# Kernel optimization log

Hardware: AMD Instinct MI355X
Metric: run time of the kernel (lower is better)

The kernel has to match this reference:

```python
import jax, jax.numpy as jnp
import numpy as np

N = 20000      # nodes
E1 = 100000    # topo (2d) edges
E2 = 100000    # distance edges
HID = 128      # hidden_size
N2D = 128      # node_embed_size_2d
E2D = 64       # edge_embed_size_2d
EF = 128       # edge_feat_size
ET = 32        # edge_type_size
NRBF = 64
CUT = 6.0


def rbf_expand(d):
    # Gaussian radial basis with cosine cutoff envelope, d: [E]
    centers = jnp.linspace(0.0, CUT, NRBF)
    width = CUT / NRBF
    env = 0.5 * (jnp.cos(jnp.pi * jnp.clip(d / CUT, 0.0, 1.0)) + 1.0)
    return jnp.exp(-((d[:, None] - centers) ** 2) / (2.0 * width * width)) * env[:, None]


def setup_inputs() -> dict:
    key = jax.random.key(0)
    ks = jax.random.split(key, 20)
    s = 0.02
    return {
        "H": jax.random.normal(ks[0], (N, HID), jnp.float32),
        "V": jax.random.normal(ks[1], (N, HID, 3), jnp.float32),
        "Z": jax.random.normal(ks[2], (N, 3), jnp.float32) * 3.0,
        "layer_i": 0,
        "H_2d": jax.random.normal(ks[3], (N, N2D), jnp.float32),
        "mask_2d": jnp.ones((N,), bool),
        "E2d_idx": jax.random.randint(ks[4], (2, E1), 0, N),
        "E2d_feat": jax.random.normal(ks[5], (E2D, E1), jnp.float32),
        "Z_3d": jax.random.normal(ks[6], (N, 3), jnp.float32) * 3.0,
        "mask_3d": jnp.ones((N,), bool),
        "Edist_idx": jax.random.randint(ks[7], (2, E2), 0, N),
        "Edist_val": jax.random.uniform(ks[8], (E2,), jnp.float32) * CUT,
        "virtual_node_embed": jax.random.normal(ks[9], (1, N2D), jnp.float32),
        "edge_type_embed": jax.random.normal(ks[10], (3, ET), jnp.float32),
        "W_rbf": jax.random.normal(ks[11], (EF, NRBF), jnp.float32) * s,
        "W_e2d": jax.random.normal(ks[12], (EF, E2D), jnp.float32) * s,
        "W_i": jax.random.normal(ks[13], (HID, HID + N2D), jnp.float32) * s,
        "W_phi1": jax.random.normal(ks[14], (HID, HID + EF + ET), jnp.float32) * s,
        "b_phi1": jnp.zeros((HID,), jnp.float32),
        "W_phi2": jax.random.normal(ks[15], (3 * HID, HID), jnp.float32) * s,
        "b_phi2": jnp.zeros((3 * HID,), jnp.float32),
        "W_msg": jax.random.normal(ks[16], (3 * HID, NRBF), jnp.float32) * s,
        "b_msg": jnp.zeros((3 * HID,), jnp.float32),
    }


def reference(H, V, Z, layer_i, H_2d, mask_2d, E2d_idx, E2d_feat, Z_3d, mask_3d,
              Edist_idx, Edist_val, virtual_node_embed, edge_type_embed,
              W_rbf, W_e2d, W_i, W_phi1, b_phi1, W_phi2, b_phi2, W_msg, b_msg):
    n = H.shape[0]
    # mask_3d is all-True in this fixture => n_cond_3d == n (static shapes)
    nodes_real = jnp.concatenate([H, H_2d], axis=-1)                       # [n, h1+h2]
    virt = jnp.broadcast_to(virtual_node_embed, (n, virtual_node_embed.shape[1]))
    nodes_virt = jnp.concatenate([H, virt], axis=-1)                        # [n, h1+h2]
    nodes = jnp.concatenate([nodes_real, nodes_virt], axis=0) @ W_i.T      # [2n, h1]
    v = jnp.concatenate([V, jnp.zeros_like(V)], axis=0)                     # [2n, h1, 3]
    z = jnp.concatenate([Z, Z_3d], axis=0)                                  # [2n, 3]

    row_3d = jnp.arange(n)
    col_3d = jnp.arange(n) + n
    E3d = jnp.stack([jnp.concatenate([row_3d, col_3d]),
                     jnp.concatenate([col_3d, row_3d])], axis=0)            # [2, 2n]
    edges = jnp.concatenate([E2d_idx, E3d, Edist_idx], axis=-1)             # [2, E]
    e1, e3, e2 = E2d_idx.shape[1], E3d.shape[1], Edist_idx.shape[1]
    edge_type = jnp.concatenate([jnp.zeros((e1,), jnp.int32),
                                 jnp.ones((e3,), jnp.int32),
                                 jnp.full((e2,), 2, jnp.int32)])
    et = edge_type_embed[edge_type]                                         # [E, ET]
    attr2d = E2d_feat.T @ W_e2d.T                                           # [e1, EF]
    attr3d = jnp.zeros((e3, W_e2d.shape[0]), jnp.float32)                   # [e3, EF]
    attrd = rbf_expand(Edist_val) @ W_rbf.T                                 # [e2, EF]
    edge_attr = jnp.concatenate(
        [jnp.concatenate([attr2d, attr3d, attrd], axis=0), et], axis=-1)    # [E, EF+ET]

    # AdapterLayer: PaiNN-style equivariant message passing
    row, col = edges[0], edges[1]
    rel = z[row] - z[col]                                                   # [E, 3]
    dist = jnp.sqrt(jnp.sum(rel * rel, axis=-1) + 1e-8)                     # [E]
    unit = rel / dist[:, None]
    phi_in = jnp.concatenate([nodes[col], edge_attr], axis=-1)
    phi = jax.nn.silu(phi_in @ W_phi1.T + b_phi1) @ W_phi2.T + b_phi2       # [E, 3h]
    wd = rbf_expand(dist) @ W_msg.T + b_msg                                 # [E, 3h]
    m = phi * wd
    h = nodes.shape[1]
    s_msg, v_gate, r_gate = m[:, :h], m[:, h:2 * h], m[:, 2 * h:]
    dv = v[col] * v_gate[:, :, None] + unit[:, None, :] * r_gate[:, :, None]  # [E, h, 3]
    nn2 = nodes.shape[0]
    H_add = jax.ops.segment_sum(s_msg, row, num_segments=nn2)[:n]
    V_add = jax.ops.segment_sum(dv, row, num_segments=nn2)[:n]

    # eval-mode clamp
    H_add = jnp.clip(H_add, -100.0, 100.0)
    V_add = jnp.clip(V_add, -100.0, 100.0)

    mask_dist = jnp.zeros((n,), bool).at[Edist_idx[0]].set(True).at[Edist_idx[1]].set(True)
    update_mask = mask_2d | mask_3d | mask_dist
    H_add = jnp.where(update_mask[:, None], H_add, 0.0)
    V_add = jnp.where(update_mask[:, None, None], V_add, 0.0)
    return H_add, V_add
```

## Files before the change

### kernel.cpp

```cpp
#include <hip/hip_runtime.h>
#include <hip/hip_bf16.h>

#define NN   20000
#define E1N  100000
#define E2N  100000
#define NEFF 220000
#define TILE 64
#define NBLK ((NEFF + TILE - 1) / TILE)
#define NPAD (NBLK * TILE)
#define RBF_STEP   0.09523809523809523f
#define RBF_INV2W2 56.88888888888889f

typedef short  bf16x8 __attribute__((ext_vector_type(8)));
typedef float  f32x4  __attribute__((ext_vector_type(4)));

__device__ __forceinline__ float4 ld4(const float* p) {
    return *reinterpret_cast<const float4*>(p);
}
__device__ __forceinline__ ushort f2bf(float x) {
    __hip_bfloat16 h = __float2bfloat16(x);
    return *reinterpret_cast<ushort*>(&h);
}
__device__ __forceinline__ float bf2f(ushort u) {
    return __uint_as_float(((unsigned)u) << 16);
}
__device__ __forceinline__ float env_of(float d) {
    float x = fminf(fmaxf(d * (1.0f / 6.0f), 0.0f), 1.0f);
    return 0.5f * (__cosf(3.14159265358979f * x) + 1.0f);
}

__device__ __forceinline__ int edge_row(int eid, const int* __restrict__ E2d_idx,
                                        const int* __restrict__ Edist_idx) {
    if (eid < E1N) return E2d_idx[eid];
    if (eid < E1N + NN) return eid - E1N;
    return Edist_idx[eid - E1N - NN];
}

__global__ __launch_bounds__(256) void hist_kernel(
    const int* __restrict__ E2d_idx, const int* __restrict__ Edist_idx,
    int* __restrict__ hist) {
    int g = blockIdx.x * 256 + threadIdx.x;
    if (g < NEFF) atomicAdd(&hist[edge_row(g, E2d_idx, Edist_idx)], 1);
}

__global__ __launch_bounds__(1024) void scan_kernel(
    const int* __restrict__ hist, int* __restrict__ start, int* __restrict__ cursor) {
    __shared__ int buf[1024];
    __shared__ int carry;
    const int t = threadIdx.x;
    if (t == 0) carry = 0;
    __syncthreads();
    for (int chunk = 0; chunk < 20; ++chunk) {
        int idx = chunk * 1024 + t;
        int v = (idx < NN) ? hist[idx] : 0;
        buf[t] = v;
        __syncthreads();
        for (int off = 1; off < 1024; off <<= 1) {
            int x = (t >= off) ? buf[t - off] : 0;
            __syncthreads();
            buf[t] += x;
            __syncthreads();
        }
        int excl  = buf[t] - v;
        int cbase = carry;
        int tot   = buf[1023];
        if (idx <= NN) {
            start[idx] = cbase + excl;
            if (idx < NN) cursor[idx] = cbase + excl;
        }
        __syncthreads();
        if (t == 0) carry = cbase + tot;
        __syncthreads();
    }
}

__global__ __launch_bounds__(256) void scatter_kernel(
    const int* __restrict__ E2d_idx, const int* __restrict__ Edist_idx,
    int* __restrict__ cursor, int* __restrict__ order) {
    int g = blockIdx.x * 256 + threadIdx.x;
    if (g < NEFF) {
        int r = edge_row(g, E2d_idx, Edist_idx);
        int pos = atomicAdd(&cursor[r], 1);
        order[pos] = g;
    }
}

__global__ __launch_bounds__(64) void chunkrow_kernel(
    const int* __restrict__ order, const int* __restrict__ E2d_idx,
    const int* __restrict__ Edist_idx, int cap, int nch, int* __restrict__ chunk_r0) {
    int i = threadIdx.x;
    if (i < nch) {
        int p = i * cap;
        if (p >= NEFF) p = NEFF - 1;
        chunk_r0[i] = edge_row(order[p], E2d_idx, Edist_idx);
    }
}

__global__ __launch_bounds__(256) void meta_kernel(
    const int* __restrict__ order, const int* __restrict__ E2d_idx,
    const int* __restrict__ Edist_idx, const float* __restrict__ Edist_val,
    const float* __restrict__ Z, const float* __restrict__ Z3d,
    int4* __restrict__ metaI, float4* __restrict__ metaF,
    float4* __restrict__ payloadU) {
    int g = blockIdx.x * 256 + threadIdx.x;
    if (g >= NPAD) return;
    int eid = (g < NEFF) ? order[g] : -1;
    int row, col, ty, e2 = 0; float dval = 0.f;
    if (eid < 0)             { ty = 1; row = -1; col = 0; }
    else if (eid < E1N)      { ty = 0; row = E2d_idx[eid]; col = E2d_idx[E1N + eid]; e2 = eid; }
    else if (eid < E1N + NN) { ty = 1; int jj = eid - E1N; row = jj; col = jj + NN; }
    else { ty = 2; int g2 = eid - E1N - NN;
           row = Edist_idx[g2]; col = Edist_idx[E2N + g2]; dval = Edist_val[g2]; }
    int rs = (row < 0) ? 0 : row;
    float prx = Z[rs * 3], pry = Z[rs * 3 + 1], prz = Z[rs * 3 + 2];
    float pcx, pcy, pcz;
    if (col < NN) { pcx = Z[col * 3]; pcy = Z[col * 3 + 1]; pcz = Z[col * 3 + 2]; }
    else { int c = col - NN; pcx = Z3d[c * 3]; pcy = Z3d[c * 3 + 1]; pcz = Z3d[c * 3 + 2]; }
    float dx = prx - pcx, dy = pry - pcy, dz = prz - pcz;
    float dist = sqrtf(dx * dx + dy * dy + dz * dz + 1e-8f);
    float inv = 1.0f / dist;
    int vcol = (col < NN) ? col : -1;
    metaI[g] = make_int4(col, row, ty, e2);
    metaF[g] = make_float4(dist, dval, env_of(dist), env_of(dval));
    if (row >= 0)
        payloadU[g] = make_float4(dx * inv, dy * inv, dz * inv, __int_as_float(vcol));
}

__global__ __launch_bounds__(256) void prep_kernel(
    const float* __restrict__ W_phi1, const float* __restrict__ b_phi1,
    const float* __restrict__ W_e2d, const float* __restrict__ W_rbf,
    const float* __restrict__ W_phi2, const float* __restrict__ W_msg,
    const float* __restrict__ et, const float* __restrict__ W_i,
    ushort* __restrict__ W1c, ushort* __restrict__ W2b,
    ushort* __restrict__ Wmb, float* __restrict__ b_type,
    ushort* __restrict__ Wib) {
    int g = blockIdx.x * 256 + threadIdx.x;
    if (g < 32768) {
        int n = g >> 8, k = g & 255;
        float v;
        if (k < 128) v = W_phi1[n * 288 + k];
        else {
            int kk = k - 128;
            const float* Wsel = (kk < 64) ? W_e2d : W_rbf;
            int j = kk & 63;
            float s = 0.f;
            for (int a = 0; a < 128; ++a) s += W_phi1[n * 288 + 128 + a] * Wsel[a * 64 + j];
            v = s;
        }
        W1c[n * 256 + k] = f2bf(v);
    } else if (g < 81920) {
        int q = g - 32768; W2b[q] = f2bf(W_phi2[q]);
    } else if (g < 106496) {
        int q = g - 81920; Wmb[q] = f2bf(W_msg[q]);
    } else if (g < 106880) {
        int q = g - 106496; int ty = q >> 7, n = q & 127;
        float s = b_phi1[n];
        for (int a = 0; a < 32; ++a) s += W_phi1[n * 288 + 256 + a] * et[ty * 32 + a];
        b_type[q] = s;
    } else if (g < 139648) {
        int q = g - 106880; Wib[q] = f2bf(W_i[q]);
    }
}

__global__ __launch_bounds__(256) void featT_kernel(
    const float* __restrict__ feat, ushort* __restrict__ featTb) {
    __shared__ float tile[64][65];
    const int t = threadIdx.x;
    const int cbase = blockIdx.x * 64;
    for (int i = t; i < 64 * 64; i += 256) {
        int k = i >> 6, e = i & 63;
        tile[k][e] = (cbase + e < E1N) ? feat[(size_t)k * E1N + cbase + e] : 0.f;
    }
    __syncthreads();
    for (int i = t; i < 64 * 64; i += 256) {
        int e = i >> 6, k = i & 63;
        if (cbase + e < E1N) featTb[(size_t)(cbase + e) * 64 + k] = f2bf(tile[k][e]);
    }
}

__global__ __launch_bounds__(256, 2) void nodes_mfma_kernel(
    const float* __restrict__ H, const float* __restrict__ H2d,
    const float* __restrict__ virt, const ushort* __restrict__ Wib,
    ushort* __restrict__ nodesb) {
    __shared__ ushort A[64][264];
    __shared__ ushort WB[128][132];

    const int t = threadIdx.x;
    const int gbase = blockIdx.x * 64;

    for (int i = t; i < 64 * 64; i += 256) {
        int e = i >> 6, q = i & 63;
        int row = gbase + e;
        float4 v;
        if (q < 32)          v = ld4(H + (size_t)((row < NN) ? row : row - NN) * 128 + q * 4);
        else if (row < NN)   v = ld4(H2d + (size_t)row * 128 + (q - 32) * 4);
        else                 v = ld4(virt + (q - 32) * 4);
        ushort tmp[4] = {f2bf(v.x), f2bf(v.y), f2bf(v.z), f2bf(v.w)};
        *reinterpret_cast<uint2*>(&A[e][q * 4]) = *reinterpret_cast<const uint2*>(tmp);
    }
    for (int i = t; i < 128 * 16; i += 256) {
        int n = i >> 4, q = i & 15;
        *reinterpret_cast<uint4*>(&WB[n][q * 8]) =
            *reinterpret_cast<const uint4*>(Wib + (size_t)n * 256 + q * 8);
    }
    __syncthreads();

    const int w  = t >> 6, lane = t & 63;
    const int mh = w >> 1, nh = w & 1;
    const int lr = lane >> 4, lc = lane & 15;
    const int ar0 = mh * 32 + lc;

    f32x4 acc[2][4];
#pragma unroll
    for (int mt = 0; mt < 2; ++mt)
#pragma unroll
        for (int nt = 0; nt < 4; ++nt) acc[mt][nt] = (f32x4){0.f, 0.f, 0.f, 0.f};
#pragma unroll
    for (int ks = 0; ks < 4; ++ks) {
        bf16x8 a0 = *reinterpret_cast<const bf16x8*>(&A[ar0][ks * 32 + lr * 8]);
        bf16x8 a1 = *reinterpret_cast<const bf16x8*>(&A[ar0 + 16][ks * 32 + lr * 8]);
#pragma unroll
        for (int nt = 0; nt < 4; ++nt) {
            int n = nh * 64 + nt * 16 + lc;
            bf16x8 b = *reinterpret_cast<const bf16x8*>(&WB[n][ks * 32 + lr * 8]);
            acc[0][nt] = __builtin_amdgcn_mfma_f32_16x16x32_bf16(a0, b, acc[0][nt], 0, 0, 0);
            acc[1][nt] = __builtin_amdgcn_mfma_f32_16x16x32_bf16(a1, b, acc[1][nt], 0, 0, 0);
        }
    }
    __syncthreads();
    for (int i = t; i < 128 * 16; i += 256) {
        int n = i >> 4, q = i & 15;
        *reinterpret_cast<uint4*>(&WB[n][q * 8]) =
            *reinterpret_cast<const uint4*>(Wib + (size_t)n * 256 + 128 + q * 8);
    }
    __syncthreads();
#pragma unroll
    for (int ks = 4; ks < 8; ++ks) {
        bf16x8 a0 = *reinterpret_cast<const bf16x8*>(&A[ar0][ks * 32 + lr * 8]);
        bf16x8 a1 = *reinterpret_cast<const bf16x8*>(&A[ar0 + 16][ks * 32 + lr * 8]);
#pragma unroll
        for (int nt = 0; nt < 4; ++nt) {
            int n = nh * 64 + nt * 16 + lc;
            bf16x8 b = *reinterpret_cast<const bf16x8*>(&WB[n][(ks - 4) * 32 + lr * 8]);
            acc[0][nt] = __builtin_amdgcn_mfma_f32_16x16x32_bf16(a0, b, acc[0][nt], 0, 0, 0);
            acc[1][nt] = __builtin_amdgcn_mfma_f32_16x16x32_bf16(a1, b, acc[1][nt], 0, 0, 0);
        }
    }
#pragma unroll
    for (int mt = 0; mt < 2; ++mt)
#pragma unroll
        for (int nt = 0; nt < 4; ++nt)
#pragma unroll
            for (int r = 0; r < 4; ++r) {
                int e  = mh * 32 + mt * 16 + lr * 4 + r;
                int ch = nh * 64 + nt * 16 + lc;
                nodesb[(size_t)(gbase + e) * 128 + ch] = f2bf(acc[mt][nt][r]);
            }
}

template <int MODE>
__global__ __launch_bounds__(256, 2) void edge_kernel(
    const ushort* __restrict__ nodesb, const float* __restrict__ V,
    const float* __restrict__ Z, const float* __restrict__ Z3d,
    const int* __restrict__ E2d_idx, const float* __restrict__ E2d_feat,
    const ushort* __restrict__ featTb,
    const int* __restrict__ Edist_idx, const float* __restrict__ Edist_val,
    const ushort* __restrict__ W1c, const ushort* __restrict__ W2b,
    const ushort* __restrict__ Wmb, const float* __restrict__ b_type,
    const float* __restrict__ b_phi2, const float* __restrict__ b_msg,
    const int4* __restrict__ metaI, const float4* __restrict__ metaF,
    int p0, ushort* __restrict__ payloadM,
    float* __restrict__ Hout, float* __restrict__ Vout) {

    __shared__ ushort A1f[TILE * 264 + 256];
    __shared__ ushort WB[128][132];
    __shared__ float  s_bt[3][128];
    __shared__ int    s_row[TILE], s_col[TILE], s_ty[TILE], s_e2[TILE], s_vcol[TILE];
    __shared__ float  s_dist[TILE], s_dval[TILE], s_env[TILE], s_env2[TILE];
    __shared__ float  s_unit[TILE][3];

    ushort* hidp  = A1f;
    ushort* m_lds = A1f + 8704;

    const int t = threadIdx.x;
    const int gbase = blockIdx.x * TILE;

    if (MODE == 1) {
        if (t < TILE) {
            int4 mi = metaI[p0 + gbase + t];
            s_col[t] = mi.x; s_row[t] = mi.y; s_ty[t] = mi.z; s_e2[t] = mi.w;
        } else if (t < 2 * TILE) {
            int e = t - TILE;
            float4 mf = metaF[p0 + gbase + e];
            s_dist[e] = mf.x; s_dval[e] = mf.y; s_env[e] = mf.z; s_env2[e] = mf.w;
        }
    } else {
        if (t < TILE) {
            int gpos = gbase + t;
            int eid = (gpos < NEFF) ? gpos : -1;
            int row, col, ty, e2 = 0; float dval = 0.f;
            if (eid < 0)             { ty = 1; row = -1; col = 0; }
            else if (eid < E1N)      { ty = 0; row = E2d_idx[eid]; col = E2d_idx[E1N + eid]; e2 = eid; }
            else if (eid < E1N + NN) { ty = 1; int jj = eid - E1N; row = jj; col = jj + NN; }
            else { ty = 2; int g2 = eid - E1N - NN;
                   row = Edist_idx[g2]; col = Edist_idx[E2N + g2]; dval = Edist_val[g2]; }
            int rs = (row < 0) ? 0 : row;
            float prx = Z[rs * 3], pry = Z[rs * 3 + 1], prz = Z[rs * 3 + 2];
            float pcx, pcy, pcz;
            if (col < NN) { pcx = Z[col * 3]; pcy = Z[col * 3 + 1]; pcz = Z[col * 3 + 2]; }
            else { int c = col - NN; pcx = Z3d[c * 3]; pcy = Z3d[c * 3 + 1]; pcz = Z3d[c * 3 + 2]; }
            float dx = prx - pcx, dy = pry - pcy, dz = prz - pcz;
            float dist = sqrtf(dx * dx + dy * dy + dz * dz + 1e-8f);
            float inv = 1.0f / dist;
            s_row[t] = row; s_col[t] = col; s_ty[t] = ty; s_e2[t] = e2;
            s_vcol[t] = (col < NN) ? col : -1;
            s_unit[t][0] = dx * inv; s_unit[t][1] = dy * inv; s_unit[t][2] = dz * inv;
            s_dist[t] = dist; s_dval[t] = dval;
            s_env[t] = env_of(dist); s_env2[t] = env_of(dval);
        }
    }
    for (int i = t; i < 384; i += 256) ((float*)s_bt)[i] = b_type[i];
    __syncthreads();

    for (int i = t; i < TILE * 16; i += 256) {
        int e = i >> 4, q = i & 15;
        *reinterpret_cast<uint4*>(&A1f[e * 264 + q * 8]) =
            *reinterpret_cast<const uint4*>(nodesb + (size_t)s_col[e] * 128 + q * 8);
    }
    if (MODE == 1) {
        for (int i = t; i < TILE * 128; i += 256) {
            int e = i >> 7, k = i & 127;
            int ty = s_ty[e];
            ushort v = 0;
            if (ty == 0) { if (k < 64) v = featTb[(size_t)s_e2[e] * 64 + k]; }
            else if (ty == 2) {
                if (k >= 64) {
                    float dd = s_dval[e] - (float)(k - 64) * RBF_STEP;
                    v = f2bf(__expf(-dd * dd * RBF_INV2W2) * s_env2[e]);
                }
            }
            A1f[e * 264 + 128 + k] = v;
        }
    } else {
        for (int i = t; i < TILE * 128; i += 256) {
            int k = i >> 6, e = i & 63;
            int ty = s_ty[e];
            float v = 0.f;
            if (ty == 0) { if (k < 64) v = E2d_feat[(size_t)k * E1N + s_e2[e]]; }
            else if (ty == 2) {
                if (k >= 64) {
                    float dd = s_dval[e] - (float)(k - 64) * RBF_STEP;
                    v = __expf(-dd * dd * RBF_INV2W2) * s_env2[e];
                }
            }
            A1f[e * 264 + 128 + k] = f2bf(v);
        }
    }
    for (int i = t; i < 128 * 16; i += 256) {
        int n = i >> 4, q = i & 15;
        *reinterpret_cast<uint4*>(&WB[n][q * 8]) =
            *reinterpret_cast<const uint4*>(W1c + (size_t)n * 256 + q * 8);
    }
    __syncthreads();

    const int w  = t >> 6, lane = t & 63;
    const int mh = w >> 1, nh = w & 1;
    const int lr = lane >> 4, lc = lane & 15;
    const int ar0 = mh * 32 + lc;

    bf16x8 ra0[2], ra1[2];
    {
        float dA = s_dist[ar0],      eA = s_env[ar0];
        float dB = s_dist[ar0 + 16], eB = s_env[ar0 + 16];
#pragma unroll
        for (int ks = 0; ks < 2; ++ks)
#pragma unroll
            for (int j = 0; j < 8; ++j) {
                float c  = (float)(ks * 32 + lr * 8 + j) * RBF_STEP;
                float tA = dA - c, tB = dB - c;
                ra0[ks][j] = (short)f2bf(__expf(-tA * tA * RBF_INV2W2) * eA);
                ra1[ks][j] = (short)f2bf(__expf(-tB * tB * RBF_INV2W2) * eB);
            }
    }

    f32x4 acc[2][4];
#pragma unroll
    for (int mt = 0; mt < 2; ++mt)
#pragma unroll
        for (int nt = 0; nt < 4; ++nt) acc[mt][nt] = (f32x4){0.f, 0.f, 0.f, 0.f};
#pragma unroll
    for (int ks = 0; ks < 4; ++ks) {
        bf16x8 a0 = *reinterpret_cast<const bf16x8*>(&A1f[ar0 * 264 + ks * 32 + lr * 8]);
        bf16x8 a1 = *reinterpret_cast<const bf16x8*>(&A1f[(ar0 + 16) * 264 + ks * 32 + lr * 8]);
#pragma unroll
        for (int nt = 0; nt < 4; ++nt) {
            int n = nh * 64 + nt * 16 + lc;
            bf16x8 b = *reinterpret_cast<const bf16x8*>(&WB[n][ks * 32 + lr * 8]);
            acc[0][nt] = __builtin_amdgcn_mfma_f32_16x16x32_bf16(a0, b, acc[0][nt], 0, 0, 0);
            acc[1][nt] = __builtin_amdgcn_mfma_f32_16x16x32_bf16(a1, b, acc[1][nt], 0, 0, 0);
        }
    }
    __syncthreads();
    for (int i = t; i < 128 * 16; i += 256) {
        int n = i >> 4, q = i & 15;
        *reinterpret_cast<uint4*>(&WB[n][q * 8]) =
            *reinterpret_cast<const uint4*>(W1c + (size_t)n * 256 + 128 + q * 8);
    }
    __syncthreads();
#pragma unroll
    for (int ks = 4; ks < 8; ++ks) {
        bf16x8 a0 = *reinterpret_cast<const bf16x8*>(&A1f[ar0 * 264 + ks * 32 + lr * 8]);
        bf16x8 a1 = *reinterpret_cast<const bf16x8*>(&A1f[(ar0 + 16) * 264 + ks * 32 + lr * 8]);
#pragma unroll
        for (int nt = 0; nt < 4; ++nt) {
            int n = nh * 64 + nt * 16 + lc;
            bf16x8 b = *reinterpret_cast<const bf16x8*>(&WB[n][(ks - 4) * 32 + lr * 8]);
            acc[0][nt] = __builtin_amdgcn_mfma_f32_16x16x32_bf16(a0, b, acc[0][nt], 0, 0, 0);
            acc[1][nt] = __builtin_amdgcn_mfma_f32_16x16x32_bf16(a1, b, acc[1][nt], 0, 0, 0);
        }
    }
    __syncthreads();

#pragma unroll
    for (int mt = 0; mt < 2; ++mt)
#pragma unroll
        for (int nt = 0; nt < 4; ++nt)
#pragma unroll
            for (int r = 0; r < 4; ++r) {
                int e  = mh * 32 + mt * 16 + lr * 4 + r;
                int ch = nh * 64 + nt * 16 + lc;
                float x = acc[mt][nt][r] + s_bt[s_ty[e]][ch];
                hidp[e * 136 + ch] = f2bf(x / (1.0f + __expf(-x)));
            }
    for (int i = t; i < 128 * 16; i += 256) {
        int n = i >> 4, q = i & 15;
        *reinterpret_cast<uint4*>(&WB[n][q * 8]) =
            *reinterpret_cast<const uint4*>(W2b + (size_t)n * 128 + q * 8);
    }
    __syncthreads();

    bf16x8 ha0[4], ha1[4];
#pragma unroll
    for (int ks = 0; ks < 4; ++ks) {
        ha0[ks] = *reinterpret_cast<const bf16x8*>(&hidp[ar0 * 136 + ks * 32 + lr * 8]);
        ha1[ks] = *reinterpret_cast<const bf16x8*>(&hidp[(ar0 + 16) * 136 + ks * 32 + lr * 8]);
    }

    f32x4 vgr[2][4];
#pragma unroll
    for (int c = 0; c < 3; ++c) {
        f32x4 p[2][4], g[2][4];
#pragma unroll
        for (int mt = 0; mt < 2; ++mt)
#pragma unroll
            for (int nt = 0; nt < 4; ++nt) {
                p[mt][nt] = (f32x4){0.f, 0.f, 0.f, 0.f};
                g[mt][nt] = (f32x4){0.f, 0.f, 0.f, 0.f};
            }
#pragma unroll
        for (int ks = 0; ks < 4; ++ks) {
#pragma unroll
            for (int nt = 0; nt < 4; ++nt) {
                int n = nh * 64 + nt * 16 + lc;
                bf16x8 b = *reinterpret_cast<const bf16x8*>(&WB[n][ks * 32 + lr * 8]);
                p[0][nt] = __builtin_amdgcn_mfma_f32_16x16x32_bf16(ha0[ks], b, p[0][nt], 0, 0, 0);
                p[1][nt] = __builtin_amdgcn_mfma_f32_16x16x32_bf16(ha1[ks], b, p[1][nt], 0, 0, 0);
            }
        }
#pragma unroll
        for (int ks = 0; ks < 2; ++ks) {
#pragma unroll
            for (int nt = 0; nt < 4; ++nt) {
                int n = c * 128 + nh * 64 + nt * 16 + lc;
                bf16x8 b = *reinterpret_cast<const bf16x8*>(Wmb + (size_t)n * 64 + ks * 32 + lr * 8);
                g[0][nt] = __builtin_amdgcn_mfma_f32_16x16x32_bf16(ra0[ks], b, g[0][nt], 0, 0, 0);
                g[1][nt] = __builtin_amdgcn_mfma_f32_16x16x32_bf16(ra1[ks], b, g[1][nt], 0, 0, 0);
            }
        }
        __syncthreads();
        if (c < 2) {
            for (int i = t; i < 128 * 16; i += 256) {
                int n = i >> 4, q = i & 15;
                *reinterpret_cast<uint4*>(&WB[n][q * 8]) =
                    *reinterpret_cast<const uint4*>(W2b + (size_t)((c + 1) * 128 + n) * 128 + q * 8);
            }
        }
#pragma unroll
        for (int mt = 0; mt < 2; ++mt)
#pragma unroll
            for (int nt = 0; nt < 4; ++nt) {
                int d  = nh * 64 + nt * 16 + lc;
                float b2 = b_phi2[c * 128 + d];
                float bm = b_msg[c * 128 + d];
#pragma unroll
                for (int r = 0; r < 4; ++r) {
                    int e = mh * 32 + mt * 16 + lr * 4 + r;
                    float m = (p[mt][nt][r] + b2) * (g[mt][nt][r] + bm);
                    if (MODE == 1) {
                        m_lds[e * 132 + d] = f2bf(m);
                    } else {
                        int row = s_row[e];
                        if (c == 0) {
                            if (row >= 0) unsafeAtomicAdd(&Hout[(size_t)row * 128 + d], m);
                        } else if (c == 1) {
                            vgr[mt][nt][r] = m;
                        } else if (row >= 0) {
                            float vgv = vgr[mt][nt][r];
                            int vc = s_vcol[e];
                            float vx = 0.f, vy = 0.f, vz = 0.f;
                            if (vc >= 0) {
                                const float* vp = V + ((size_t)vc * 128 + d) * 3;
                                vx = vp[0]; vy = vp[1]; vz = vp[2];
                            }
                            float* vo = Vout + ((size_t)row * 128 + d) * 3;
                            unsafeAtomicAdd(vo + 0, vx * vgv + s_unit[e][0] * m);
                            unsafeAtomicAdd(vo + 1, vy * vgv + s_unit[e][1] * m);
                            unsafeAtomicAdd(vo + 2, vz * vgv + s_unit[e][2] * m);
                        }
                    }
                }
            }
        __syncthreads();
        if (MODE == 1) {
            for (int i = t; i < 2048; i += 256) {
                int e = i >> 5, q = i & 31;
                *reinterpret_cast<uint2*>(payloadM + (size_t)(gbase + e) * 384 + c * 128 + q * 4) =
                    *reinterpret_cast<const uint2*>(m_lds + e * 132 + q * 4);
            }
        }
    }
}

__global__ __launch_bounds__(256) void reduce_kernel(
    const ushort* __restrict__ payloadM, const float4* __restrict__ payloadU,
    const float* __restrict__ V, const int* __restrict__ start,
    const int* __restrict__ chunk_r0, int ci, int p0, int p1,
    float* __restrict__ Hout, float* __restrict__ Vout) {
    const int t = threadIdx.x;
    const int rbase = chunk_r0[ci] + blockIdx.x * 8;
    const bool hside = (t < 128);
    const int d = hside ? t : (t - 128);
    for (int nr = 0; nr < 8; ++nr) {
        int r = rbase + nr;
        if (r >= NN) return;
        int s0 = start[r], s1 = start[r + 1];
        if (s0 >= p1) return;
        int a = (s0 > p0) ? s0 : p0;
        int b = (s1 < p1) ? s1 : p1;
        if (a >= b) continue;
        int n = b - a;
        if (hside) {
            const ushort* base = payloadM + (size_t)(a - p0) * 384 + d;
            float a0 = 0.f, a1 = 0.f, a2 = 0.f, a3 = 0.f;
            int i = 0;
            for (; i + 4 <= n; i += 4) {
                a0 += bf2f(base[(size_t)i * 384]);
                a1 += bf2f(base[(size_t)(i + 1) * 384]);
                a2 += bf2f(base[(size_t)(i + 2) * 384]);
                a3 += bf2f(base[(size_t)(i + 3) * 384]);
            }
            for (; i < n; ++i) a0 += bf2f(base[(size_t)i * 384]);
            float acc = (a0 + a1) + (a2 + a3);
            float* ptr = &Hout[(size_t)r * 128 + d];
            float o = *ptr + acc;
            if (s1 <= p1) o = fminf(fmaxf(o, -100.f), 100.f);
            *ptr = o;
        } else {
            const ushort* base = payloadM + (size_t)(a - p0) * 384;
            const float4* ub = payloadU + a;
            float ax = 0.f, ay = 0.f, az = 0.f;
            float bx = 0.f, by = 0.f, bz = 0.f;
            int i = 0;
            for (; i + 2 <= n; i += 2) {
                const ushort* pm0 = base + (size_t)i * 384;
                const ushort* pm1 = base + (size_t)(i + 1) * 384;
                float vg0 = bf2f(pm0[128 + d]), rg0 = bf2f(pm0[256 + d]);
                float vg1 = bf2f(pm1[128 + d]), rg1 = bf2f(pm1[256 + d]);
                float4 u0 = ub[i];
                float4 u1 = ub[i + 1];
                int vc0 = __float_as_int(u0.w);
                int vc1 = __float_as_int(u1.w);
                if (vc0 >= 0) {
                    const float* vp = V + (size_t)vc0 * 384 + d * 3;
                    ax += vg0 * vp[0]; ay += vg0 * vp[1]; az += vg0 * vp[2];
                }
                if (vc1 >= 0) {
                    const float* vp = V + (size_t)vc1 * 384 + d * 3;
                    bx += vg1 * vp[0]; by += vg1 * vp[1]; bz += vg1 * vp[2];
                }
                ax += rg0 * u0.x; ay += rg0 * u0.y; az += rg0 * u0.z;
                bx += rg1 * u1.x; by += rg1 * u1.y; bz += rg1 * u1.z;
            }
            if (i < n) {
                const ushort* pm0 = base + (size_t)i * 384;
                float vg0 = bf2f(pm0[128 + d]), rg0 = bf2f(pm0[256 + d]);
                float4 u0 = ub[i];
                int vc0 = __float_as_int(u0.w);
                if (vc0 >= 0) {
                    const float* vp = V + (size_t)vc0 * 384 + d * 3;
                    ax += vg0 * vp[0]; ay += vg0 * vp[1]; az += vg0 * vp[2];
                }
                ax += rg0 * u0.x; ay += rg0 * u0.y; az += rg0 * u0.z;
            }
            ax += bx; ay += by; az += bz;
            float* vo = Vout + (size_t)r * 384 + d * 3;
            float ox = vo[0] + ax, oy = vo[1] + ay, oz = vo[2] + az;
            if (s1 <= p1) {
                ox = fminf(fmaxf(ox, -100.f), 100.f);
                oy = fminf(fmaxf(oy, -100.f), 100.f);
                oz = fminf(fmaxf(oz, -100.f), 100.f);
            }
            vo[0] = ox; vo[1] = oy; vo[2] = oz;
        }
    }
}

extern "C" void kernel_launch(void* const* d_in, const int* in_sizes, int n_in,
                              void* d_out, int out_size, void* d_ws, size_t ws_size,
                              hipStream_t stream) {
    const float* H         = (const float*)d_in[0];
    const float* V         = (const float*)d_in[1];
    const float* Z         = (const float*)d_in[2];
    const float* H2d       = (const float*)d_in[4];
    const int*   E2d_idx   = (const int*)d_in[6];
    const float* E2d_feat  = (const float*)d_in[7];
    const float* Z3d       = (const float*)d_in[8];
    const int*   Edist_idx = (const int*)d_in[10];
    const float* Edist_val = (const float*)d_in[11];
    const float* virt      = (const float*)d_in[12];
    const float* et        = (const float*)d_in[13];
    const float* W_rbf     = (const float*)d_in[14];
    const float* W_e2d     = (const float*)d_in[15];
    const float* W_i       = (const float*)d_in[16];
    const float* W_phi1    = (const float*)d_in[17];
    const float* b_phi1    = (const float*)d_in[18];
    const float* W_phi2    = (const float*)d_in[19];
    const float* b_phi2    = (const float*)d_in[20];
    const float* W_msg     = (const float*)d_in[21];
    const float* b_msg     = (const float*)d_in[22];

    ushort* nodesb  = (ushort*)d_ws;
    ushort* W1c     = nodesb + 5120000;
    ushort* W2b     = W1c + 32768;
    ushort* Wmb     = W2b + 49152;
    ushort* Wib     = Wmb + 24576;
    float*  b_type  = (float*)(Wib + 32768);
    ushort* featTb  = (ushort*)(b_type + 384);
    int*    hist    = (int*)(featTb + (size_t)E1N * 64);
    int*    cursor  = hist + NN;
    int*    start   = cursor + NN;
    int*    order   = start + NN + 1;
    int*    chunk_r0= order + NPAD;
    int4*   metaI   = (int4*)(((size_t)(chunk_r0 + 64) + 15) & ~(size_t)15);
    float4* metaF   = (float4*)(metaI + NPAD);
    float4* payloadU= metaF + NPAD;

    size_t fixed = (size_t)((char*)(payloadU + NPAD) - (char*)d_ws);
    size_t poff  = (fixed + 255) & ~(size_t)255;
    size_t avail = (ws_size > poff) ? (ws_size - poff) : 0;
    long long cap_ll = (long long)(avail / 768) / TILE * TILE;
    int cap = (cap_ll > (long long)NPAD) ? NPAD : (int)cap_ll;
    const bool big = (cap >= 4096);
    ushort* payloadM = (ushort*)((char*)d_ws + poff);

    float* Hout = (float*)d_out;
    float* Vout = Hout + (size_t)NN * 128;

    hipMemsetAsync(d_out, 0, (size_t)out_size * sizeof(float), stream);
    prep_kernel<<<(139648 + 255) / 256, 256, 0, stream>>>(
        W_phi1, b_phi1, W_e2d, W_rbf, W_phi2, W_msg, et, W_i,
        W1c, W2b, Wmb, b_type, Wib);
    nodes_mfma_kernel<<<(2 * NN) / 64, 256, 0, stream>>>(H, H2d, virt, Wib, nodesb);

    if (big) {
        hipMemsetAsync(hist, 0, NN * sizeof(int), stream);
        featT_kernel<<<(E1N + 63) / 64, 256, 0, stream>>>(E2d_feat, featTb);
        hist_kernel<<<(NEFF + 255) / 256, 256, 0, stream>>>(E2d_idx, Edist_idx, hist);
        scan_kernel<<<1, 1024, 0, stream>>>(hist, start, cursor);
        scatter_kernel<<<(NEFF + 255) / 256, 256, 0, stream>>>(E2d_idx, Edist_idx, cursor, order);
        meta_kernel<<<(NPAD + 255) / 256, 256, 0, stream>>>(
            order, E2d_idx, Edist_idx, Edist_val, Z, Z3d, metaI, metaF, payloadU);
        int bpc = cap / TILE;
        int nch = (NBLK + bpc - 1) / bpc;
        chunkrow_kernel<<<1, 64, 0, stream>>>(order, E2d_idx, Edist_idx, cap, nch, chunk_r0);
        int rbound = (NN < cap + 1) ? NN : (cap + 1);
        int rgrid  = (rbound + 7) / 8;
        for (int ci = 0; ci < nch; ++ci) {
            int b0 = ci * bpc;
            int nb = ((NBLK - b0) < bpc) ? (NBLK - b0) : bpc;
            int p0 = b0 * TILE;
            int p1 = p0 + nb * TILE; if (p1 > NEFF) p1 = NEFF;
            edge_kernel<1><<<nb, 256, 0, stream>>>(
                nodesb, V, Z, Z3d, E2d_idx, E2d_feat, featTb, Edist_idx, Edist_val,
                W1c, W2b, Wmb, b_type, b_phi2, b_msg, metaI, metaF, p0, payloadM,
                Hout, Vout);
            reduce_kernel<<<rgrid, 256, 0, stream>>>(payloadM, payloadU, V, start,
                                                     chunk_r0, ci, p0, p1, Hout, Vout);
        }
    } else {
        edge_kernel<0><<<NBLK, 256, 0, stream>>>(
            nodesb, V, Z, Z3d, E2d_idx, E2d_feat, featTb, Edist_idx, Edist_val,
            W1c, W2b, Wmb, b_type, b_phi2, b_msg, metaI, metaF, 0, payloadM,
            Hout, Vout);
    }
}
```

Before: 405.2 us.

## Fuse segmented row reduction into edge kernel, drop payload buffer and reduce pass

The separate reduce_kernel and its chunk loop are removed. The edge kernel now sums messages for consecutive same-row edges inside each sorted tile, reading from LDS planes. It writes a row directly when the row lies entirely within the tile and uses atomics at tile boundaries. This avoids writing and re-reading a large bf16 message payload in global memory and removes many kernel launches. The cost is serial per-thread reduction loops run by only half the block, and rows that span tiles are accumulated by atomics without the final clamp.

Result: slower. 512.5 us (+26.5%).

```diff
diff --git a/kernel.cpp b/kernel.cpp
--- a/kernel.cpp
+++ b/kernel.cpp
@@ -27,6 +27,9 @@
 __device__ __forceinline__ float env_of(float d) {
     float x = fminf(fmaxf(d * (1.0f / 6.0f), 0.0f), 1.0f);
     return 0.5f * (__cosf(3.14159265358979f * x) + 1.0f);
+}
+__device__ __forceinline__ float clip100(float x) {
+    return fminf(fmaxf(x, -100.f), 100.f);
 }
 
 __device__ __forceinline__ int edge_row(int eid, const int* __restrict__ E2d_idx,
@@ -85,23 +88,12 @@
     }
 }
 
-__global__ __launch_bounds__(64) void chunkrow_kernel(
-    const int* __restrict__ order, const int* __restrict__ E2d_idx,
-    const int* __restrict__ Edist_idx, int cap, int nch, int* __restrict__ chunk_r0) {
-    int i = threadIdx.x;
-    if (i < nch) {
-        int p = i * cap;
-        if (p >= NEFF) p = NEFF - 1;
-        chunk_r0[i] = edge_row(order[p], E2d_idx, Edist_idx);
-    }
-}
-
 __global__ __launch_bounds__(256) void meta_kernel(
     const int* __restrict__ order, const int* __restrict__ E2d_idx,
     const int* __restrict__ Edist_idx, const float* __restrict__ Edist_val,
     const float* __restrict__ Z, const float* __restrict__ Z3d,
     int4* __restrict__ metaI, float4* __restrict__ metaF,
-    float4* __restrict__ payloadU) {
+    float4* __restrict__ metaU) {
     int g = blockIdx.x * 256 + threadIdx.x;
     if (g >= NPAD) return;
     int eid = (g < NEFF) ? order[g] : -1;
@@ -122,8 +114,9 @@
     int vcol = (col < NN) ? col : -1;
     metaI[g] = make_int4(col, row, ty, e2);
     metaF[g] = make_float4(dist, dval, env_of(dist), env_of(dval));
-    if (row >= 0)
-        payloadU[g] = make_float4(dx * inv, dy * inv, dz * inv, __int_as_float(vcol));
+    metaU[g] = (row >= 0)
+        ? make_float4(dx * inv, dy * inv, dz * inv, __int_as_float(vcol))
+        : make_float4(0.f, 0.f, 0.f, __int_as_float(-1));
 }
 
 __global__ __launch_bounds__(256) void prep_kernel(
@@ -269,7 +262,7 @@
     const ushort* __restrict__ Wmb, const float* __restrict__ b_type,
     const float* __restrict__ b_phi2, const float* __restrict__ b_msg,
     const int4* __restrict__ metaI, const float4* __restrict__ metaF,
-    int p0, ushort* __restrict__ payloadM,
+    const float4* __restrict__ metaU, const int* __restrict__ start,
     float* __restrict__ Hout, float* __restrict__ Vout) {
 
     __shared__ ushort A1f[TILE * 264 + 256];
@@ -279,19 +272,24 @@
     __shared__ float  s_dist[TILE], s_dval[TILE], s_env[TILE], s_env2[TILE];
     __shared__ float  s_unit[TILE][3];
 
-    ushort* hidp  = A1f;
-    ushort* m_lds = A1f + 8704;
+    ushort* hidp   = A1f;
+    ushort* plane0 = A1f;
+    ushort* plane1 = A1f + 8448;
 
     const int t = threadIdx.x;
     const int gbase = blockIdx.x * TILE;
+    const int pg = gbase;
 
     if (MODE == 1) {
         if (t < TILE) {
-            int4 mi = metaI[p0 + gbase + t];
+            int4 mi = metaI[gbase + t];
             s_col[t] = mi.x; s_row[t] = mi.y; s_ty[t] = mi.z; s_e2[t] = mi.w;
+            float4 u = metaU[gbase + t];
+            s_unit[t][0] = u.x; s_unit[t][1] = u.y; s_unit[t][2] = u.z;
+            s_vcol[t] = __float_as_int(u.w);
         } else if (t < 2 * TILE) {
             int e = t - TILE;
-            float4 mf = metaF[p0 + gbase + e];
+            float4 mf = metaF[gbase + e];
             s_dist[e] = mf.x; s_dval[e] = mf.y; s_env[e] = mf.z; s_env2[e] = mf.w;
         }
     } else {
@@ -478,27 +476,130 @@
             }
         }
         __syncthreads();
-        if (c < 2) {
-            for (int i = t; i < 128 * 16; i += 256) {
-                int n = i >> 4, q = i & 15;
-                *reinterpret_cast<uint4*>(&WB[n][q * 8]) =
-                    *reinterpret_cast<const uint4*>(W2b + (size_t)((c + 1) * 128 + n) * 128 + q * 8);
-            }
-        }
-#pragma unroll
-        for (int mt = 0; mt < 2; ++mt)
-#pragma unroll
-            for (int nt = 0; nt < 4; ++nt) {
-                int d  = nh * 64 + nt * 16 + lc;
-                float b2 = b_phi2[c * 128 + d];
-                float bm = b_msg[c * 128 + d];
-#pragma unroll
-                for (int r = 0; r < 4; ++r) {
-                    int e = mh * 32 + mt * 16 + lr * 4 + r;
-                    float m = (p[mt][nt][r] + b2) * (g[mt][nt][r] + bm);
-                    if (MODE == 1) {
-                        m_lds[e * 132 + d] = f2bf(m);
-                    } else {
+
+        if (MODE == 1) {
+            ushort* dst = (c == 1) ? plane1 : plane0;
+#pragma unroll
+            for (int mt = 0; mt < 2; ++mt)
+#pragma unroll
+                for (int nt = 0; nt < 4; ++nt) {
+                    int d  = nh * 64 + nt * 16 + lc;
+                    float b2 = b_phi2[c * 128 + d];
+                    float bm = b_msg[c * 128 + d];
+#pragma unroll
+                    for (int r = 0; r < 4; ++r) {
+                        int e = mh * 32 + mt * 16 + lr * 4 + r;
+                        dst[e * 132 + d] = f2bf((p[mt][nt][r] + b2) * (g[mt][nt][r] + bm));
+                    }
+                }
+            if (c == 1) {
+                for (int i = t; i < 128 * 16; i += 256) {
+                    int n = i >> 4, q = i & 15;
+                    *reinterpret_cast<uint4*>(&WB[n][q * 8]) =
+                        *reinterpret_cast<const uint4*>(W2b + (size_t)(256 + n) * 128 + q * 8);
+                }
+            }
+            __syncthreads();
+
+            if (c == 0) {
+                if (t < 128) {
+                    const int d = t;
+                    float a0 = 0.f; int cur = -2, e0 = 0;
+                    for (int e = 0; e < TILE; ++e) {
+                        int row = s_row[e];
+                        if (row != cur) {
+                            if (cur >= 0) {
+                                bool ib = (e0 > 0) || (start[cur] == pg);
+                                bool ie = true;
+                                (void)ie;
+                                if (ib) Hout[(size_t)cur * 128 + d] = clip100(a0);
+                                else    unsafeAtomicAdd(&Hout[(size_t)cur * 128 + d], a0);
+                            }
+                            cur = row; e0 = e; a0 = 0.f;
+                        }
+                        if (cur >= 0) a0 += bf2f(plane0[e * 132 + d]);
+                    }
+                    if (cur >= 0) {
+                        bool ib = (e0 > 0) || (start[cur] == pg);
+                        bool ie = (start[cur + 1] == pg + TILE);
+                        if (ib && ie) Hout[(size_t)cur * 128 + d] = clip100(a0);
+                        else          unsafeAtomicAdd(&Hout[(size_t)cur * 128 + d], a0);
+                    }
+                } else {
+                    for (int i = t - 128; i < 128 * 16; i += 128) {
+                        int n = i >> 4, q = i & 15;
+                        *reinterpret_cast<uint4*>(&WB[n][q * 8]) =
+                            *reinterpret_cast<const uint4*>(W2b + (size_t)(128 + n) * 128 + q * 8);
+                    }
+                }
+                __syncthreads();
+            } else if (c == 2) {
+                if (t < 128) {
+                    const int d = t;
+                    float ax = 0.f, ay = 0.f, az = 0.f;
+                    int cur = -2, e0 = 0;
+                    for (int e = 0; e < TILE; ++e) {
+                        int row = s_row[e];
+                        if (row != cur) {
+                            if (cur >= 0) {
+                                bool ib = (e0 > 0) || (start[cur] == pg);
+                                float* vo = Vout + (size_t)cur * 384 + d * 3;
+                                if (ib) {
+                                    vo[0] = clip100(ax); vo[1] = clip100(ay); vo[2] = clip100(az);
+                                } else {
+                                    unsafeAtomicAdd(vo + 0, ax);
+                                    unsafeAtomicAdd(vo + 1, ay);
+                                    unsafeAtomicAdd(vo + 2, az);
+                                }
+                            }
+                            cur = row; e0 = e; ax = ay = az = 0.f;
+                        }
+                        if (cur >= 0) {
+                            float vg = bf2f(plane1[e * 132 + d]);
+                            float rg = bf2f(plane0[e * 132 + d]);
+                            int vc = s_vcol[e];
+                            if (vc >= 0) {
+                                const float* vp = V + (size_t)vc * 384 + d * 3;
+                                ax += vg * vp[0]; ay += vg * vp[1]; az += vg * vp[2];
+                            }
+                            ax += rg * s_unit[e][0];
+                            ay += rg * s_unit[e][1];
+                            az += rg * s_unit[e][2];
+                        }
+                    }
+                    if (cur >= 0) {
+                        bool ib = (e0 > 0) || (start[cur] == pg);
+                        bool ie = (start[cur + 1] == pg + TILE);
+                        float* vo = Vout + (size_t)cur * 384 + d * 3;
+                        if (ib && ie) {
+                            vo[0] = clip100(ax); vo[1] = clip100(ay); vo[2] = clip100(az);
+                        } else {
+                            unsafeAtomicAdd(vo + 0, ax);
+                            unsafeAtomicAdd(vo + 1, ay);
+                            unsafeAtomicAdd(vo + 2, az);
+                        }
+                    }
+                }
+            }
+        } else {
+            if (c < 2) {
+                for (int i = t; i < 128 * 16; i += 256) {
+                    int n = i >> 4, q = i & 15;
+                    *reinterpret_cast<uint4*>(&WB[n][q * 8]) =
+                        *reinterpret_cast<const uint4*>(W2b + (size_t)((c + 1) * 128 + n) * 128 + q * 8);
+                }
+            }
+#pragma unroll
+            for (int mt = 0; mt < 2; ++mt)
+#pragma unroll
+                for (int nt = 0; nt < 4; ++nt) {
+                    int d  = nh * 64 + nt * 16 + lc;
+                    float b2 = b_phi2[c * 128 + d];
+                    float bm = b_msg[c * 128 + d];
+#pragma unroll
+                    for (int r = 0; r < 4; ++r) {
+                        int e = mh * 32 + mt * 16 + lr * 4 + r;
+                        float m = (p[mt][nt][r] + b2) * (g[mt][nt][r] + bm);
                         int row = s_row[e];
                         if (c == 0) {
                             if (row >= 0) unsafeAtomicAdd(&Hout[(size_t)row * 128 + d], m);
@@ -519,98 +620,7 @@
                         }
                     }
                 }
-            }
-        __syncthreads();
-        if (MODE == 1) {
-            for (int i = t; i < 2048; i += 256) {
-                int e = i >> 5, q = i & 31;
-                *reinterpret_cast<uint2*>(payloadM + (size_t)(gbase + e) * 384 + c * 128 + q * 4) =
-                    *reinterpret_cast<const uint2*>(m_lds + e * 132 + q * 4);
-            }
-        }
-    }
-}
-
-__global__ __launch_bounds__(256) void reduce_kernel(
-    const ushort* __restrict__ payloadM, const float4* __restrict__ payloadU,
-    const float* __restrict__ V, const int* __restrict__ start,
-    const int* __restrict__ chunk_r0, int ci, int p0, int p1,
-    float* __restrict__ Hout, float* __restrict__ Vout) {
-    const int t = threadIdx.x;
-    const int rbase = chunk_r0[ci] + blockIdx.x * 8;
-    const bool hside = (t < 128);
-    const int d = hside ? t : (t - 128);
-    for (int nr = 0; nr < 8; ++nr) {
-        int r = rbase + nr;
-        if (r >= NN) return;
-        int s0 = start[r], s1 = start[r + 1];
-        if (s0 >= p1) return;
-        int a = (s0 > p0) ? s0 : p0;
-        int b = (s1 < p1) ? s1 : p1;
-        if (a >= b) continue;
-        int n = b - a;
-        if (hside) {
-            const ushort* base = payloadM + (size_t)(a - p0) * 384 + d;
-            float a0 = 0.f, a1 = 0.f, a2 = 0.f, a3 = 0.f;
-            int i = 0;
-            for (; i + 4 <= n; i += 4) {
-                a0 += bf2f(base[(size_t)i * 384]);
-                a1 += bf2f(base[(size_t)(i + 1) * 384]);
-                a2 += bf2f(base[(size_t)(i + 2) * 384]);
-                a3 += bf2f(base[(size_t)(i + 3) * 384]);
-            }
-            for (; i < n; ++i) a0 += bf2f(base[(size_t)i * 384]);
-            float acc = (a0 + a1) + (a2 + a3);
-            float* ptr = &Hout[(size_t)r * 128 + d];
-            float o = *ptr + acc;
-            if (s1 <= p1) o = fminf(fmaxf(o, -100.f), 100.f);
-            *ptr = o;
-        } else {
-            const ushort* base = payloadM + (size_t)(a - p0) * 384;
-            const float4* ub = payloadU + a;
-            float ax = 0.f, ay = 0.f, az = 0.f;
-            float bx = 0.f, by = 0.f, bz = 0.f;
-            int i = 0;
-            for (; i + 2 <= n; i += 2) {
-                const ushort* pm0 = base + (size_t)i * 384;
-                const ushort* pm1 = base + (size_t)(i + 1) * 384;
-                float vg0 = bf2f(pm0[128 + d]), rg0 = bf2f(pm0[256 + d]);
-                float vg1 = bf2f(pm1[128 + d]), rg1 = bf2f(pm1[256 + d]);
-                float4 u0 = ub[i];
-                float4 u1 = ub[i + 1];
-                int vc0 = __float_as_int(u0.w);
-                int vc1 = __float_as_int(u1.w);
-                if (vc0 >= 0) {
-                    const float* vp = V + (size_t)vc0 * 384 + d * 3;
-                    ax += vg0 * vp[0]; ay += vg0 * vp[1]; az += vg0 * vp[2];
-                }
-                if (vc1 >= 0) {
-                    const float* vp = V + (size_t)vc1 * 384 + d * 3;
-                    bx += vg1 * vp[0]; by += vg1 * vp[1]; bz += vg1 * vp[2];
-                }
-                ax += rg0 * u0.x; ay += rg0 * u0.y; az += rg0 * u0.z;
-                bx += rg1 * u1.x; by += rg1 * u1.y; bz += rg1 * u1.z;
-            }
-            if (i < n) {
-                const ushort* pm0 = base + (size_t)i * 384;
-                float vg0 = bf2f(pm0[128 + d]), rg0 = bf2f(pm0[256 + d]);
-                float4 u0 = ub[i];
-                int vc0 = __float_as_int(u0.w);
-                if (vc0 >= 0) {
-                    const float* vp = V + (size_t)vc0 * 384 + d * 3;
-                    ax += vg0 * vp[0]; ay += vg0 * vp[1]; az += vg0 * vp[2];
-                }
-                ax += rg0 * u0.x; ay += rg0 * u0.y; az += rg0 * u0.z;
-            }
-            ax += bx; ay += by; az += bz;
-            float* vo = Vout + (size_t)r * 384 + d * 3;
-            float ox = vo[0] + ax, oy = vo[1] + ay, oz = vo[2] + az;
-            if (s1 <= p1) {
-                ox = fminf(fmaxf(ox, -100.f), 100.f);
-                oy = fminf(fmaxf(oy, -100.f), 100.f);
-                oz = fminf(fmaxf(oz, -100.f), 100.f);
-            }
-            vo[0] = ox; vo[1] = oy; vo[2] = oz;
+            __syncthreads();
         }
     }
 }
@@ -650,18 +660,12 @@
     int*    cursor  = hist + NN;
     int*    start   = cursor + NN;
     int*    order   = start + NN + 1;
-    int*    chunk_r0= order + NPAD;
-    int4*   metaI   = (int4*)(((size_t)(chunk_r0 + 64) + 15) & ~(size_t)15);
+    int4*   metaI   = (int4*)(((size_t)(order + NPAD) + 15) & ~(size_t)15);
     float4* metaF   = (float4*)(metaI + NPAD);
-    float4* payloadU= metaF + NPAD;
-
-    size_t fixed = (size_t)((char*)(payloadU + NPAD) - (char*)d_ws);
-    size_t poff  = (fixed + 255) & ~(size_t)255;
-    size_t avail = (ws_size > poff) ? (ws_size - poff) : 0;
-    long long cap_ll = (long long)(avail / 768) / TILE * TILE;
-    int cap = (cap_ll > (long long)NPAD) ? NPAD : (int)cap_ll;
-    const bool big = (cap >= 4096);
-    ushort* payloadM = (ushort*)((char*)d_ws + poff);
+    float4* metaU   = metaF + NPAD;
+
+    size_t fixed = (size_t)((char*)(metaU + NPAD) - (char*)d_ws);
+    const bool big = (ws_size >= fixed);
 
     float* Hout = (float*)d_out;
     float* Vout = Hout + (size_t)NN * 128;
@@ -679,28 +683,15 @@
         scan_kernel<<<1, 1024, 0, stream>>>(hist, start, cursor);
         scatter_kernel<<<(NEFF + 255) / 256, 256, 0, stream>>>(E2d_idx, Edist_idx, cursor, order);
         meta_kernel<<<(NPAD + 255) / 256, 256, 0, stream>>>(
-            order, E2d_idx, Edist_idx, Edist_val, Z, Z3d, metaI, metaF, payloadU);
-        int bpc = cap / TILE;
-        int nch = (NBLK + bpc - 1) / bpc;
-        chunkrow_kernel<<<1, 64, 0, stream>>>(order, E2d_idx, Edist_idx, cap, nch, chunk_r0);
-        int rbound = (NN < cap + 1) ? NN : (cap + 1);
-        int rgrid  = (rbound + 7) / 8;
-        for (int ci = 0; ci < nch; ++ci) {
-            int b0 = ci * bpc;
-            int nb = ((NBLK - b0) < bpc) ? (NBLK - b0) : bpc;
-            int p0 = b0 * TILE;
-            int p1 = p0 + nb * TILE; if (p1 > NEFF) p1 = NEFF;
-            edge_kernel<1><<<nb, 256, 0, stream>>>(
-                nodesb, V, Z, Z3d, E2d_idx, E2d_feat, featTb, Edist_idx, Edist_val,
-                W1c, W2b, Wmb, b_type, b_phi2, b_msg, metaI, metaF, p0, payloadM,
-                Hout, Vout);
-            reduce_kernel<<<rgrid, 256, 0, stream>>>(payloadM, payloadU, V, start,
-                                                     chunk_r0, ci, p0, p1, Hout, Vout);
-        }
+            order, E2d_idx, Edist_idx, Edist_val, Z, Z3d, metaI, metaF, metaU);
+        edge_kernel<1><<<NBLK, 256, 0, stream>>>(
+            nodesb, V, Z, Z3d, E2d_idx, E2d_feat, featTb, Edist_idx, Edist_val,
+            W1c, W2b, Wmb, b_type, b_phi2, b_msg, metaI, metaF, metaU, start,
+            Hout, Vout);
     } else {
         edge_kernel<0><<<NBLK, 256, 0, stream>>>(
             nodesb, V, Z, Z3d, E2d_idx, E2d_feat, featTb, Edist_idx, Edist_val,
-            W1c, W2b, Wmb, b_type, b_phi2, b_msg, metaI, metaF, 0, payloadM,
+            W1c, W2b, Wmb, b_type, b_phi2, b_msg, metaI, metaF, metaU, start,
             Hout, Vout);
     }
 }
```
